# Optimization experiments

Measured on AMD Instinct MI355X. Metric: run time of the kernel, lower is better.

Reference implementation:

```python
import jax, jax.numpy as jnp
import numpy as np

B, L_IN, C_IN, C_SKIP, C_OUT, DEPTH = 8, 512, 512, 512, 512, 4
D_INNER, D_STATE, D_CONV, DT_RANK = 1024, 16, 4, 32
EPS = 1e-5


def rmsnorm(x, w):
    return x * jax.lax.rsqrt(jnp.mean(x * x, axis=-1, keepdims=True) + EPS) * w


def layernorm(x, w, b):
    m = jnp.mean(x, axis=-1, keepdims=True)
    v = jnp.mean((x - m) ** 2, axis=-1, keepdims=True)
    return (x - m) * jax.lax.rsqrt(v + EPS) * w + b


def selective_scan(u, dt, A, Bm, Cm, Dp):
    # u, dt: (B, L, Di); A: (Di, N); Bm, Cm: (B, L, N); Dp: (Di,)
    def step(h, inp):
        dt_t, B_t, C_t, u_t = inp  # (B,Di),(B,N),(B,N),(B,Di)
        dA = jnp.exp(dt_t[..., None] * A)            # (B,Di,N)
        h = dA * h + (dt_t * u_t)[..., None] * B_t[:, None, :]
        y = jnp.einsum('bdn,bn->bd', h, C_t)
        return h, y

    Bb, L, Di = u.shape
    h0 = jnp.zeros((Bb, Di, A.shape[1]), u.dtype)
    xs = (dt.transpose(1, 0, 2), Bm.transpose(1, 0, 2),
          Cm.transpose(1, 0, 2), u.transpose(1, 0, 2))
    _, ys = jax.lax.scan(step, h0, xs)               # ys: (L,B,Di)
    return ys.transpose(1, 0, 2) + u * Dp


def mamba_block(x, in_w, cw, cb, xp_w, dtw, dtb, A_log, Dp, ow, ob):
    xz = x @ in_w.T                                   # (B,L,2*Di)
    xc, z = jnp.split(xz, 2, axis=-1)
    # causal depthwise conv, kernel D_CONV
    xc_t = jax.lax.conv_general_dilated(
        xc.transpose(0, 2, 1), cw[:, None, :], (1,), [(D_CONV - 1, 0)],
        feature_group_count=D_INNER,
        dimension_numbers=('NCH', 'OIH', 'NCH'))
    xc = jax.nn.silu((xc_t + cb[None, :, None]).transpose(0, 2, 1))
    xdbc = xc @ xp_w.T                                # (B,L,DT_RANK+2N)
    dtp = xdbc[..., :DT_RANK]
    Bm = xdbc[..., DT_RANK:DT_RANK + D_STATE]
    Cm = xdbc[..., DT_RANK + D_STATE:]
    dt = jax.nn.softplus(dtp @ dtw.T + dtb)
    A = -jnp.exp(A_log)
    y = selective_scan(xc, dt, A, Bm, Cm, Dp)
    return (y * jax.nn.silu(z)) @ ow.T + ob


def forward(motion_input, skip_feats, embed, w_up, b_up, w1, b1, rms_w, w2, b2,
            ln_w, ln_b, in_proj_w, conv_w, conv_b, x_proj_w, dt_proj_w,
            dt_proj_b, A_log, D_param, out_proj_w, out_proj_b,
            norm_f_w, norm_f_b):
    Bb, Lin, C = motion_input.shape
    # ConvTranspose1d(C, C, kernel=2, stride=2): non-overlapping expansion
    up = jnp.einsum('blc,cok->blko', motion_input, w_up)
    up = up.reshape(Bb, Lin * 2, C) + b_up            # (B, 2L, C)
    x = jnp.concatenate([up, skip_feats], axis=-1)    # (B, 2L, C+skip)
    # MLP: Linear -> RMSNorm -> SiLU -> Linear
    x = jax.nn.silu(rmsnorm(x @ w1.T + b1, rms_w)) @ w2.T + b2
    # MotionMamba: add embed, depth residual mamba blocks, final norm
    x = x + embed[:, None, :]
    for i in range(DEPTH):
        x = x + mamba_block(layernorm(x, ln_w[i], ln_b[i]), in_proj_w[i],
                            conv_w[i], conv_b[i], x_proj_w[i], dt_proj_w[i],
                            dt_proj_b[i], A_log[i], D_param[i],
                            out_proj_w[i], out_proj_b[i])
    return layernorm(x, norm_f_w, norm_f_b)


def setup_inputs():
    key = jax.random.key(0)
    ks = jax.random.split(key, 16)
    f = lambda k, sh: jax.random.normal(k, sh, jnp.float32) * 0.02
    inp = {}
    inp['motion_input'] = jax.random.normal(ks[0], (B, L_IN, C_IN), jnp.float32)
    inp['skip_feats'] = jax.random.normal(ks[1], (B, 2 * L_IN, C_SKIP), jnp.float32)
    inp['embed'] = jax.random.normal(ks[2], (B, C_OUT), jnp.float32)
    inp['w_up'] = f(ks[3], (C_IN, C_IN, 2))
    inp['b_up'] = jnp.zeros((C_IN,), jnp.float32)
    inp['w1'] = f(ks[4], (C_OUT, C_IN + C_SKIP))
    inp['b1'] = jnp.zeros((C_OUT,), jnp.float32)
    inp['rms_w'] = jnp.ones((C_OUT,), jnp.float32)
    inp['w2'] = f(ks[5], (C_OUT, C_OUT))
    inp['b2'] = jnp.zeros((C_OUT,), jnp.float32)
    inp['ln_w'] = jnp.ones((DEPTH, C_OUT), jnp.float32)
    inp['ln_b'] = jnp.zeros((DEPTH, C_OUT), jnp.float32)
    inp['in_proj_w'] = f(ks[6], (DEPTH, 2 * D_INNER, C_OUT))
    inp['conv_w'] = f(ks[7], (DEPTH, D_INNER, D_CONV))
    inp['conv_b'] = jnp.zeros((DEPTH, D_INNER), jnp.float32)
    inp['x_proj_w'] = f(ks[8], (DEPTH, DT_RANK + 2 * D_STATE, D_INNER))
    inp['dt_proj_w'] = f(ks[9], (DEPTH, D_INNER, DT_RANK))
    inp['dt_proj_b'] = jnp.full((DEPTH, D_INNER), -4.0, jnp.float32)
    inp['A_log'] = jnp.log(jnp.tile(jnp.arange(1, D_STATE + 1, dtype=jnp.float32), (DEPTH, D_INNER, 1)))
    inp['D_param'] = jnp.ones((DEPTH, D_INNER), jnp.float32)
    inp['out_proj_w'] = f(ks[10], (DEPTH, C_OUT, D_INNER))
    inp['out_proj_b'] = jnp.zeros((DEPTH, C_OUT), jnp.float32)
    inp['norm_f_w'] = jnp.ones((C_OUT,), jnp.float32)
    inp['norm_f_b'] = jnp.zeros((C_OUT,), jnp.float32)
    return inp


def reference(motion_input, skip_feats, embed, w_up, b_up, w1, b1, rms_w, w2,
              b2, ln_w, ln_b, in_proj_w, conv_w, conv_b, x_proj_w, dt_proj_w,
              dt_proj_b, A_log, D_param, out_proj_w, out_proj_b,
              norm_f_w, norm_f_b):
    return forward(motion_input, skip_feats, embed, w_up, b_up, w1, b1, rms_w,
                   w2, b2, ln_w, ln_b, in_proj_w, conv_w, conv_b, x_proj_w,
                   dt_proj_w, dt_proj_b, A_log, D_param, out_proj_w,
                   out_proj_b, norm_f_w, norm_f_b)
```

## Files before the change

kernel.cpp:

```cpp
#include <hip/hip_runtime.h>
#include <cstdint>
#include <cstddef>

#define DEV_INLINE __device__ __forceinline__

static constexpr float EPS = 1e-5f;

DEV_INLINE float sigmoidf_(float x) { return 1.0f / (1.0f + __expf(-x)); }
DEV_INLINE float siluf_(float x) { return x * sigmoidf_(x); }
DEV_INLINE float softplus_fast(float x) {
    return fmaxf(x, 0.0f) + __logf(1.0f + __expf(-fabsf(x)));
}
DEV_INLINE unsigned short f2bf(float x) {
    unsigned u = __builtin_bit_cast(unsigned, x);
    u += 0x7FFFu + ((u >> 16) & 1u);
    return (unsigned short)(u >> 16);
}
DEV_INLINE float bf2f(unsigned short s) {
    unsigned u = ((unsigned)s) << 16;
    return __builtin_bit_cast(float, u);
}

typedef __attribute__((ext_vector_type(8))) short bf16x8;
typedef __attribute__((ext_vector_type(4))) float f32x4;

DEV_INLINE void gload16(const unsigned short* src, char* ldsdst) {
    __builtin_amdgcn_global_load_lds(
        (const __attribute__((address_space(1))) unsigned int*)src,
        (__attribute__((address_space(3))) unsigned int*)ldsdst, 16, 0, 0);
}

DEV_INLINE void cvt8(const float* __restrict__ s, unsigned short* __restrict__ d, int t) {
    float4 f0 = *(const float4*)(s + (size_t)t * 8);
    float4 f1 = *(const float4*)(s + (size_t)t * 8 + 4);
    union { unsigned short u[8]; uint4 v; } pk;
    pk.u[0] = f2bf(f0.x); pk.u[1] = f2bf(f0.y); pk.u[2] = f2bf(f0.z); pk.u[3] = f2bf(f0.w);
    pk.u[4] = f2bf(f1.x); pk.u[5] = f2bf(f1.y); pk.u[6] = f2bf(f1.z); pk.u[7] = f2bf(f1.w);
    *(uint4*)(d + (size_t)t * 8) = pk.v;
}

__global__ __launch_bounds__(256) void prep_all(
    const float* __restrict__ motion, const float* __restrict__ wup,
    const float* __restrict__ w1, const float* __restrict__ w2,
    const float* __restrict__ in_proj_w, const float* __restrict__ out_proj_w,
    const float* __restrict__ x_proj_w, const float* __restrict__ dt_proj_w,
    unsigned short* __restrict__ mbf, unsigned short* __restrict__ wupT,
    unsigned short* __restrict__ w1b, unsigned short* __restrict__ w2b,
    unsigned short* __restrict__ lw)
{
    int bid = (int)blockIdx.x, tid = (int)threadIdx.x;
    if (bid < 1024) {
        cvt8(motion, mbf, bid * 256 + tid);
    } else if (bid < 2048) {
        int t = (bid - 1024) * 256 + tid;
        int c = t >> 9, o = t & 511;
        float2 v = *(const float2*)(wup + (size_t)t * 2);
        wupT[(size_t)o * 512 + c] = f2bf(v.x);
        wupT[262144 + (size_t)o * 512 + c] = f2bf(v.y);
    } else if (bid < 2304) {
        cvt8(w1, w1b, (bid - 2048) * 256 + tid);
    } else if (bid < 2432) {
        cvt8(w2, w2b, (bid - 2304) * 256 + tid);
    } else {
        int r = bid - 2432;
        int layer = r / 816;
        int lb = r - layer * 816;
        unsigned short* base = lw + (size_t)layer * 1671168;
        if (lb < 512) {
            cvt8(in_proj_w + (size_t)layer * 1048576, base, lb * 256 + tid);
        } else if (lb < 768) {
            cvt8(out_proj_w + (size_t)layer * 524288, base + 1048576,
                 (lb - 512) * 256 + tid);
        } else if (lb < 800) {
            cvt8(x_proj_w + (size_t)layer * 65536, base + 1572864,
                 (lb - 768) * 256 + tid);
        } else {
            cvt8(dt_proj_w + (size_t)layer * 32768, base + 1638400,
                 (lb - 800) * 256 + tid);
        }
    }
}

template <int ACT, bool ACC, bool EMBED, bool OBF>
__global__ __launch_bounds__(256) void gemm_mfma(
    const unsigned short* __restrict__ A, int lda,
    const unsigned short* __restrict__ W, int ldw,
    void* __restrict__ Cv, int ldc, int N, int K, int gx,
    const float* __restrict__ bias, const float* __restrict__ embed)
{
    __shared__ unsigned short Asm[2][128 * 64];
    __shared__ unsigned short Wsm[2][128 * 64];
    const int tid = (int)threadIdx.x;
    const int lane = tid & 63;
    const int wv = tid >> 6;
    const int wm = wv >> 1, wn = wv & 1;

    const int nwg = (int)gridDim.x;
    const int lin = (int)blockIdx.x;
    const int logical = (lin & 7) * (nwg >> 3) + (lin >> 3);
    const int by = logical / gx;
    const int bx = logical - by * gx;
    const int bm = by * 128, bn = bx * 128;

    f32x4 acc[4][4] = {};
    const int l8 = lane >> 3;
    const int wc = lane & 7;
    const int wcg = wc ^ l8;
    const int NT = K >> 6;

    {
        char* aB = (char*)Asm[0];
        char* bB = (char*)Wsm[0];
#pragma unroll
        for (int i = 0; i < 4; ++i) {
            int rb = (i * 4 + wv) * 8;
            gload16(W + (size_t)(bn + rb + l8) * ldw + wcg * 8, bB + rb * 128);
            gload16(A + (size_t)(bm + rb + l8) * lda + wcg * 8, aB + rb * 128);
        }
    }
    __syncthreads();

    for (int t = 0; t < NT; ++t) {
        const int cur = t & 1;
        if (t + 1 < NT) {
            const int k1 = (t + 1) << 6;
            char* aB = (char*)Asm[cur ^ 1];
            char* bB = (char*)Wsm[cur ^ 1];
#pragma unroll
            for (int i = 0; i < 4; ++i) {
                int rb = (i * 4 + wv) * 8;
                gload16(W + (size_t)(bn + rb + l8) * ldw + k1 + wcg * 8, bB + rb * 128);
                gload16(A + (size_t)(bm + rb + l8) * lda + k1 + wcg * 8, aB + rb * 128);
            }
        }
        const char* aB = (const char*)Asm[cur];
        const char* bB = (const char*)Wsm[cur];
        const int rA = wm * 64 + (lane & 15);
        const int rB = wn * 64 + (lane & 15);
        const int q = lane >> 4;
#pragma unroll
        for (int kk = 0; kk < 2; ++kk) {
            bf16x8 af[4], bfr[4];
#pragma unroll
            for (int mi = 0; mi < 4; ++mi) {
                int row = rA + mi * 16;
                int ch = (kk * 4 + q) ^ (row & 7);
                af[mi] = *(const bf16x8*)(aB + row * 128 + ch * 16);
            }
#pragma unroll
            for (int ni = 0; ni < 4; ++ni) {
                int row = rB + ni * 16;
                int ch = (kk * 4 + q) ^ (row & 7);
                bfr[ni] = *(const bf16x8*)(bB + row * 128 + ch * 16);
            }
#pragma unroll
            for (int mi = 0; mi < 4; ++mi)
#pragma unroll
                for (int ni = 0; ni < 4; ++ni)
                    acc[mi][ni] = __builtin_amdgcn_mfma_f32_16x16x32_bf16(
                        af[mi], bfr[ni], acc[mi][ni], 0, 0, 0);
        }
        __syncthreads();
    }

    const int cn = lane & 15;
    const int r0 = (lane >> 4) * 4;
    const int eb = EMBED ? (bm >> 10) * N : 0;
#pragma unroll
    for (int ni = 0; ni < 4; ++ni) {
        int col = bn + wn * 64 + ni * 16 + cn;
        float add = bias ? bias[col] : 0.0f;
        if (EMBED) add += embed[eb + col];
#pragma unroll
        for (int mi = 0; mi < 4; ++mi) {
#pragma unroll
            for (int r = 0; r < 4; ++r) {
                int row = bm + wm * 64 + mi * 16 + r0 + r;
                float v = acc[mi][ni][r] + add;
                if (ACT == 1) v = softplus_fast(v);
                if (OBF) {
                    ((unsigned short*)Cv)[(size_t)row * ldc + col] = f2bf(v);
                } else {
                    float* p = (float*)Cv + (size_t)row * ldc + col;
                    if (ACC) *p += v; else *p = v;
                }
            }
        }
    }
}

template <int ACT, bool ACC, bool EMBED, bool OBF, bool UPS>
__global__ __launch_bounds__(256) void gemm_mfma64(
    const unsigned short* __restrict__ A, int lda,
    const unsigned short* __restrict__ W, int ldw,
    void* __restrict__ Cv, int ldc, int N, int K, int gx,
    const float* __restrict__ bias, const float* __restrict__ embed)
{
    __shared__ unsigned short Asm[2][64 * 64];
    __shared__ unsigned short Wsm[2][64 * 64];
    const int tid = (int)threadIdx.x;
    const int lane = tid & 63;
    const int wv = tid >> 6;
    const int wm = wv >> 1, wn = wv & 1;

    const int nwg = (int)gridDim.x;
    const int lin = (int)blockIdx.x;
    const int logical = (lin & 7) * (nwg >> 3) + (lin >> 3);
    const int by = logical / gx;
    const int bx = logical - by * gx;
    const int bm = by * 64, bn = bx * 64;

    f32x4 acc[2][2] = {};
    const int l8 = lane >> 3;
    const int wc = lane & 7;
    const int wcg = wc ^ l8;
    const int NT = K >> 6;

    {
        char* aB = (char*)Asm[0];
        char* bB = (char*)Wsm[0];
#pragma unroll
        for (int i = 0; i < 2; ++i) {
            int rb = (i * 4 + wv) * 8;
            gload16(W + (size_t)(bn + rb + l8) * ldw + wcg * 8, bB + rb * 128);
            gload16(A + (size_t)(bm + rb + l8) * lda + wcg * 8, aB + rb * 128);
        }
    }
    __syncthreads();

    for (int t = 0; t < NT; ++t) {
        const int cur = t & 1;
        if (t + 1 < NT) {
            const int k1 = (t + 1) << 6;
            char* aB = (char*)Asm[cur ^ 1];
            char* bB = (char*)Wsm[cur ^ 1];
#pragma unroll
            for (int i = 0; i < 2; ++i) {
                int rb = (i * 4 + wv) * 8;
                gload16(W + (size_t)(bn + rb + l8) * ldw + k1 + wcg * 8, bB + rb * 128);
                gload16(A + (size_t)(bm + rb + l8) * lda + k1 + wcg * 8, aB + rb * 128);
            }
        }
        const char* aB = (const char*)Asm[cur];
        const char* bB = (const char*)Wsm[cur];
        const int rA = wm * 32 + (lane & 15);
        const int rB = wn * 32 + (lane & 15);
        const int q = lane >> 4;
#pragma unroll
        for (int kk = 0; kk < 2; ++kk) {
            bf16x8 af[2], bfr[2];
#pragma unroll
            for (int mi = 0; mi < 2; ++mi) {
                int row = rA + mi * 16;
                int ch = (kk * 4 + q) ^ (row & 7);
                af[mi] = *(const bf16x8*)(aB + row * 128 + ch * 16);
            }
#pragma unroll
            for (int ni = 0; ni < 2; ++ni) {
                int row = rB + ni * 16;
                int ch = (kk * 4 + q) ^ (row & 7);
                bfr[ni] = *(const bf16x8*)(bB + row * 128 + ch * 16);
            }
#pragma unroll
            for (int mi = 0; mi < 2; ++mi)
#pragma unroll
                for (int ni = 0; ni < 2; ++ni)
                    acc[mi][ni] = __builtin_amdgcn_mfma_f32_16x16x32_bf16(
                        af[mi], bfr[ni], acc[mi][ni], 0, 0, 0);
        }
        __syncthreads();
    }

    const int cn = lane & 15;
    const int r0 = (lane >> 4) * 4;
    const int eb = EMBED ? (bm >> 10) * N : 0;
#pragma unroll
    for (int ni = 0; ni < 2; ++ni) {
        int col = bn + wn * 32 + ni * 16 + cn;
        float add = bias ? bias[UPS ? (col & 511) : col] : 0.0f;
        if (EMBED) add += embed[eb + col];
#pragma unroll
        for (int mi = 0; mi < 2; ++mi) {
#pragma unroll
            for (int r = 0; r < 4; ++r) {
                int row = bm + wm * 32 + mi * 16 + r0 + r;
                float v = acc[mi][ni][r] + add;
                if (ACT == 1) v = softplus_fast(v);
                if (UPS) {
                    size_t ad = (size_t)row * 2048 + ((col >> 9) << 10) + (col & 511);
                    ((unsigned short*)Cv)[ad] = f2bf(v);
                } else if (OBF) {
                    ((unsigned short*)Cv)[(size_t)row * ldc + col] = f2bf(v);
                } else {
                    float* p = (float*)Cv + (size_t)row * ldc + col;
                    if (ACC) *p += v; else *p = v;
                }
            }
        }
    }
}

__global__ __launch_bounds__(256) void gemm_dt(
    const unsigned short* __restrict__ xdbc,
    const unsigned short* __restrict__ wdt,
    const float* __restrict__ bias,
    unsigned short* __restrict__ out)
{
    __shared__ unsigned short S[128 * 136];
    const int tid = (int)threadIdx.x;
    const int lane = tid & 63;
    const int wv = tid >> 6;
    const int wm = wv >> 1, wn = wv & 1;

    const int lin = (int)blockIdx.x;
    const int logical = (lin & 7) * 64 + (lin >> 3);
    const int bm = (logical >> 3) * 128;
    const int bn = (logical & 7) * 128;

    const int fr = lane & 15;
    const int q = lane >> 4;

    bf16x8 af[4], wf[4];
#pragma unroll
    for (int mi = 0; mi < 4; ++mi)
        af[mi] = *(const bf16x8*)(xdbc + (size_t)(bm + wm * 64 + mi * 16 + fr) * 64 + q * 8);
#pragma unroll
    for (int ni = 0; ni < 4; ++ni)
        wf[ni] = *(const bf16x8*)(wdt + (size_t)(bn + wn * 64 + ni * 16 + fr) * 32 + q * 8);

    f32x4 acc[4][4] = {};
#pragma unroll
    for (int mi = 0; mi < 4; ++mi)
#pragma unroll
        for (int ni = 0; ni < 4; ++ni)
            acc[mi][ni] = __builtin_amdgcn_mfma_f32_16x16x32_bf16(
                af[mi], wf[ni], acc[mi][ni], 0, 0, 0);

    const int cn = lane & 15;
    const int r0 = (lane >> 4) * 4;
#pragma unroll
    for (int ni = 0; ni < 4; ++ni) {
        int lcol = wn * 64 + ni * 16 + cn;
        float add = bias[bn + lcol];
#pragma unroll
        for (int mi = 0; mi < 4; ++mi) {
#pragma unroll
            for (int r = 0; r < 4; ++r) {
                int lrow = wm * 64 + mi * 16 + r0 + r;
                S[lrow * 136 + lcol] = f2bf(softplus_fast(acc[mi][ni][r] + add));
            }
        }
    }
    __syncthreads();

    const int row = tid >> 1;
    const int half = tid & 1;
    const unsigned short* src = S + row * 136 + half * 64;
    unsigned short* dst = out + (size_t)(bm + row) * 1024 + bn + half * 64;
#pragma unroll
    for (int k = 0; k < 8; ++k) {
        uint4 v = *(const uint4*)(src + k * 8);
        *(uint4*)(dst + k * 8) = v;
    }
}

__global__ __launch_bounds__(128) void gemm_xdbc(
    const unsigned short* __restrict__ A,
    const unsigned short* __restrict__ W,
    unsigned short* __restrict__ C)
{
    __shared__ unsigned short Asm[64 * 64];
    __shared__ unsigned short Wsm[64 * 64];
    const int tid = (int)threadIdx.x;
    const int lane = tid & 63;
    const int w = tid >> 6;
    const int bm = blockIdx.x * 64;
    const int l8 = lane >> 3, wc = lane & 7, wcg = wc ^ l8;
    char* aB = (char*)Asm;
    char* bB = (char*)Wsm;

    f32x4 acc[2][4] = {};

    for (int k0 = 0; k0 < 1024; k0 += 64) {
#pragma unroll
        for (int i = 0; i < 4; ++i) {
            int rb = (i * 2 + w) * 8;
            gload16(A + (size_t)(bm + rb + l8) * 1024 + k0 + wcg * 8, aB + rb * 128);
            gload16(W + (size_t)(rb + l8) * 1024 + k0 + wcg * 8, bB + rb * 128);
        }
        __syncthreads();
        const int rA = w * 32 + (lane & 15);
        const int rB = (lane & 15);
        const int q = lane >> 4;
#pragma unroll
        for (int kk = 0; kk < 2; ++kk) {
            bf16x8 af[2], bfr[4];
#pragma unroll
            for (int mi = 0; mi < 2; ++mi) {
                int row = rA + mi * 16;
                int ch = (kk * 4 + q) ^ (row & 7);
                af[mi] = *(const bf16x8*)(aB + row * 128 + ch * 16);
            }
#pragma unroll
            for (int ni = 0; ni < 4; ++ni) {
                int row = rB + ni * 16;
                int ch = (kk * 4 + q) ^ (row & 7);
                bfr[ni] = *(const bf16x8*)(bB + row * 128 + ch * 16);
            }
#pragma unroll
            for (int mi = 0; mi < 2; ++mi)
#pragma unroll
                for (int ni = 0; ni < 4; ++ni)
                    acc[mi][ni] = __builtin_amdgcn_mfma_f32_16x16x32_bf16(
                        af[mi], bfr[ni], acc[mi][ni], 0, 0, 0);
        }
        __syncthreads();
    }
    const int cn = lane & 15;
    const int r0 = (lane >> 4) * 4;
#pragma unroll
    for (int mi = 0; mi < 2; ++mi)
#pragma unroll
        for (int ni = 0; ni < 4; ++ni)
#pragma unroll
            for (int r = 0; r < 4; ++r) {
                int row = bm + w * 32 + mi * 16 + r0 + r;
                C[(size_t)row * 64 + ni * 16 + cn] = f2bf(acc[mi][ni][r]);
            }
}

__global__ __launch_bounds__(256) void concat_skip(
    const float* __restrict__ skip, unsigned short* __restrict__ x0)
{
    int t = blockIdx.x * 256 + (int)threadIdx.x;
    int row = t >> 6;
    int c8 = (t & 63) << 3;
    const float* s = skip + (size_t)row * 512 + c8;
    float4 f0 = *(const float4*)s;
    float4 f1 = *(const float4*)(s + 4);
    union { unsigned short u[8]; uint4 v; } pk;
    pk.u[0] = f2bf(f0.x); pk.u[1] = f2bf(f0.y); pk.u[2] = f2bf(f0.z); pk.u[3] = f2bf(f0.w);
    pk.u[4] = f2bf(f1.x); pk.u[5] = f2bf(f1.y); pk.u[6] = f2bf(f1.z); pk.u[7] = f2bf(f1.w);
    *(uint4*)(x0 + (size_t)row * 1024 + 512 + c8) = pk.v;
}

template <bool BFOUT>
__global__ __launch_bounds__(256) void layernorm_k(
    const float* __restrict__ x, void* __restrict__ outp,
    const float* __restrict__ w, const float* __restrict__ b)
{
    const int row = blockIdx.x * 4 + ((int)threadIdx.x >> 6);
    const int lane = (int)threadIdx.x & 63;
    const float* xr = x + (size_t)row * 512;
    float4 v0 = *(const float4*)(xr + lane * 4);
    float4 v1 = *(const float4*)(xr + 256 + lane * 4);
    float s = v0.x + v0.y + v0.z + v0.w + v1.x + v1.y + v1.z + v1.w;
    float q = v0.x*v0.x + v0.y*v0.y + v0.z*v0.z + v0.w*v0.w
            + v1.x*v1.x + v1.y*v1.y + v1.z*v1.z + v1.w*v1.w;
#pragma unroll
    for (int o = 32; o; o >>= 1) {
        s += __shfl_xor(s, o, 64);
        q += __shfl_xor(q, o, 64);
    }
    const float mean = s * (1.0f / 512.0f);
    const float var = q * (1.0f / 512.0f) - mean * mean;
    const float rstd = rsqrtf(var + EPS);
    float4 w0 = *(const float4*)(w + lane * 4);
    float4 w1 = *(const float4*)(w + 256 + lane * 4);
    float4 b0 = *(const float4*)(b + lane * 4);
    float4 b1 = *(const float4*)(b + 256 + lane * 4);
    float4 o0, o1;
    o0.x = (v0.x - mean) * rstd * w0.x + b0.x;
    o0.y = (v0.y - mean) * rstd * w0.y + b0.y;
    o0.z = (v0.z - mean) * rstd * w0.z + b0.z;
    o0.w = (v0.w - mean) * rstd * w0.w + b0.w;
    o1.x = (v1.x - mean) * rstd * w1.x + b1.x;
    o1.y = (v1.y - mean) * rstd * w1.y + b1.y;
    o1.z = (v1.z - mean) * rstd * w1.z + b1.z;
    o1.w = (v1.w - mean) * rstd * w1.w + b1.w;
    if (BFOUT) {
        unsigned short* ob = (unsigned short*)outp + (size_t)row * 512;
        union { unsigned short u[4]; uint2 v; } p0, p1;
        p0.u[0] = f2bf(o0.x); p0.u[1] = f2bf(o0.y); p0.u[2] = f2bf(o0.z); p0.u[3] = f2bf(o0.w);
        p1.u[0] = f2bf(o1.x); p1.u[1] = f2bf(o1.y); p1.u[2] = f2bf(o1.z); p1.u[3] = f2bf(o1.w);
        *(uint2*)(ob + lane * 4) = p0.v;
        *(uint2*)(ob + 256 + lane * 4) = p1.v;
    } else {
        float* orow = (float*)outp + (size_t)row * 512;
        *(float4*)(orow + lane * 4) = o0;
        *(float4*)(orow + 256 + lane * 4) = o1;
    }
}

__global__ __launch_bounds__(256) void rms_silu_k(
    const float* __restrict__ x, unsigned short* __restrict__ o,
    const float* __restrict__ w)
{
    const int row = blockIdx.x * 4 + ((int)threadIdx.x >> 6);
    const int lane = (int)threadIdx.x & 63;
    const float* xr = x + (size_t)row * 512;
    float4 v0 = *(const float4*)(xr + lane * 4);
    float4 v1 = *(const float4*)(xr + 256 + lane * 4);
    float q = v0.x*v0.x + v0.y*v0.y + v0.z*v0.z + v0.w*v0.w
            + v1.x*v1.x + v1.y*v1.y + v1.z*v1.z + v1.w*v1.w;
#pragma unroll
    for (int of = 32; of; of >>= 1) q += __shfl_xor(q, of, 64);
    const float scale = rsqrtf(q * (1.0f / 512.0f) + EPS);
    float4 w0 = *(const float4*)(w + lane * 4);
    float4 w1 = *(const float4*)(w + 256 + lane * 4);
    union { unsigned short u[4]; uint2 v; } p0, p1;
    p0.u[0] = f2bf(siluf_(v0.x * scale * w0.x));
    p0.u[1] = f2bf(siluf_(v0.y * scale * w0.y));
    p0.u[2] = f2bf(siluf_(v0.z * scale * w0.z));
    p0.u[3] = f2bf(siluf_(v0.w * scale * w0.w));
    p1.u[0] = f2bf(siluf_(v1.x * scale * w1.x));
    p1.u[1] = f2bf(siluf_(v1.y * scale * w1.y));
    p1.u[2] = f2bf(siluf_(v1.z * scale * w1.z));
    p1.u[3] = f2bf(siluf_(v1.w * scale * w1.w));
    unsigned short* ob = o + (size_t)row * 512;
    *(uint2*)(ob + lane * 4) = p0.v;
    *(uint2*)(ob + 256 + lane * 4) = p1.v;
}

__global__ __launch_bounds__(256) void conv_silu_k2(
    const unsigned short* __restrict__ xz, unsigned short* __restrict__ ub,
    const float* __restrict__ cw, const float* __restrict__ cb)
{
    int t = blockIdx.x * 256 + (int)threadIdx.x;
    int d = t & 1023;
    int bc = t >> 10;
    int b = bc >> 4, ch = bc & 15;
    int l0 = ch * 64;
    float4 w4 = *(const float4*)(cw + (size_t)d * 4);
    float bias = cb[d];
    const unsigned short* src = xz + ((size_t)(b * 1024 + l0)) * 2048 + d;
    unsigned short* dst = ub + ((size_t)(b * 1024 + l0)) * 1024 + d;
    float x0 = 0.f, x1 = 0.f, x2 = 0.f;
    if (l0 > 0) {
        x0 = bf2f(src[-(size_t)3 * 2048]);
        x1 = bf2f(src[-(size_t)2 * 2048]);
        x2 = bf2f(src[-(size_t)1 * 2048]);
    }
    for (int l = 0; l < 64; ++l) {
        float x3 = bf2f(src[(size_t)l * 2048]);
        float v = fmaf(x0, w4.x, fmaf(x1, w4.y, fmaf(x2, w4.z, fmaf(x3, w4.w, bias))));
        dst[(size_t)l * 1024] = f2bf(siluf_(v));
        x0 = x1; x1 = x2; x2 = x3;
    }
}

template <int CTRL>
DEV_INLINE float dpp_f(float x) {
    int yi = __builtin_amdgcn_update_dpp(
        0, __builtin_bit_cast(int, x), CTRL, 0xF, 0xF, true);
    return __builtin_bit_cast(float, yi);
}

template <int PHASE>
__global__ __launch_bounds__(256) void scan6(
    const unsigned short* __restrict__ dtp,
    const unsigned short* ubf,
    unsigned short* ybf,
    const unsigned short* __restrict__ xdbc,
    const unsigned short* __restrict__ zbf,
    float* __restrict__ hp,
    const float* __restrict__ A_log,
    const float* __restrict__ Dp)
{
    __shared__ float SDT[64 * 68];
    __shared__ float SB[32][20];
    __shared__ float SC[PHASE == 2 ? 32 : 1][20];
    __shared__ float YS[PHASE == 2 ? 32 : 1][68];

    const int lin = (int)blockIdx.x;
    const int logical = (lin & 7) * 128 + (lin >> 3);
    const int gg = logical & 15;
    const int r = logical >> 4;
    const int c = r & 7, b = r >> 3;
    if (PHASE == 1 && c == 7) return;
    const int tid = (int)threadIdx.x;
    const int dl = tid >> 2, qq = tid & 3;
    const int wv = tid >> 6;
    const int lane = tid & 63;
    const int dblk = gg << 6;
    const int d = dblk + dl;
    const int m0 = b * 1024 + c * 128;

    float An[4];
#pragma unroll
    for (int j = 0; j < 4; ++j)
        An[j] = -__expf(A_log[(size_t)d * 16 + qq * 4 + j]);

    float h[4] = {};
    float prod[4] = {1.f, 1.f, 1.f, 1.f};
    if (PHASE == 2) {
        const float* hpb = hp + ((size_t)(b * 1024 + d)) * 256 + qq * 8;
        for (int cc = 0; cc < c; ++cc) {
            float4 v0 = *(const float4*)(hpb + cc * 32);
            float4 v1 = *(const float4*)(hpb + cc * 32 + 4);
            h[0] = fmaf(v0.y, h[0], v0.x);
            h[1] = fmaf(v0.w, h[1], v0.z);
            h[2] = fmaf(v1.y, h[2], v1.x);
            h[3] = fmaf(v1.w, h[3], v1.z);
        }
    }

    const int bcr = (tid & 127) >> 2;
    const int bne = (tid & 3) << 2;

    unsigned short rdt0[4], rdt1[4], ru0[4], ru1[4];
    uint2 rBC;

#pragma unroll
    for (int j = 0; j < 4; ++j) {
        size_t r0 = (size_t)(m0 + 2 * (wv * 4 + j));
        rdt0[j] = dtp[r0 * 1024 + dblk + lane];
        rdt1[j] = dtp[(r0 + 1) * 1024 + dblk + lane];
        ru0[j]  = ubf[r0 * 1024 + dblk + lane];
        ru1[j]  = ubf[(r0 + 1) * 1024 + dblk + lane];
    }
    if (tid < 128) {
        rBC = *(const uint2*)(xdbc + (size_t)(m0 + bcr) * 64 + 32 + bne);
    } else if (PHASE == 2) {
        rBC = *(const uint2*)(xdbc + (size_t)(m0 + bcr) * 64 + 48 + bne);
    }

    for (int s = 0; s < 4; ++s) {
        const int lbase = s * 32;
        if (PHASE == 1 && s > 0) __syncthreads();
#pragma unroll
        for (int j = 0; j < 4; ++j) {
            float d0 = bf2f(rdt0[j]), d1 = bf2f(rdt1[j]);
            float4 wvv = {d0, d0 * bf2f(ru0[j]), d1, d1 * bf2f(ru1[j])};
            *(float4*)&SDT[lane * 68 + (wv * 4 + j) * 4] = wvv;
        }
        if (tid < 128) {
            const unsigned short* bb = (const unsigned short*)&rBC;
            float4 bv = {bf2f(bb[0]), bf2f(bb[1]), bf2f(bb[2]), bf2f(bb[3])};
            *(float4*)&SB[bcr][bne] = bv;
        } else if (PHASE == 2) {
            const unsigned short* cc2 = (const unsigned short*)&rBC;
            float4 cv = {bf2f(cc2[0]), bf2f(cc2[1]), bf2f(cc2[2]), bf2f(cc2[3])};
            *(float4*)&SC[bcr][bne] = cv;
        }
        if (s < 3) {
            const int nb = lbase + 32;
#pragma unroll
            for (int j = 0; j < 4; ++j) {
                size_t r0 = (size_t)(m0 + nb + 2 * (wv * 4 + j));
                rdt0[j] = dtp[r0 * 1024 + dblk + lane];
                rdt1[j] = dtp[(r0 + 1) * 1024 + dblk + lane];
                ru0[j]  = ubf[r0 * 1024 + dblk + lane];
                ru1[j]  = ubf[(r0 + 1) * 1024 + dblk + lane];
            }
            if (tid < 128) {
                rBC = *(const uint2*)(xdbc + (size_t)(m0 + nb + bcr) * 64 + 32 + bne);
            } else if (PHASE == 2) {
                rBC = *(const uint2*)(xdbc + (size_t)(m0 + nb + bcr) * 64 + 48 + bne);
            }
        }
        __syncthreads();

        for (int l2 = 0; l2 < 16; ++l2) {
            float4 sd = *(const float4*)&SDT[dl * 68 + l2 * 4];
            float4 B0 = *(const float4*)&SB[2 * l2][qq * 4];
            float4 B1 = *(const float4*)&SB[2 * l2 + 1][qq * 4];
            float p0 = 0.0f, p1 = 0.0f;
            float4 C0, C1;
            if (PHASE == 2) {
                C0 = *(const float4*)&SC[2 * l2][qq * 4];
                C1 = *(const float4*)&SC[2 * l2 + 1][qq * 4];
            }
            const float* B0p = (const float*)&B0;
            const float* B1p = (const float*)&B1;
            const float* C0p = (const float*)&C0;
            const float* C1p = (const float*)&C1;
#pragma unroll
            for (int j = 0; j < 4; ++j) {
                float e0 = __expf(sd.x * An[j]);
                if (PHASE == 1) prod[j] *= e0;
                h[j] = fmaf(e0, h[j], sd.y * B0p[j]);
                if (PHASE == 2) p0 = fmaf(h[j], C0p[j], p0);
                float e1 = __expf(sd.z * An[j]);
                if (PHASE == 1) prod[j] *= e1;
                h[j] = fmaf(e1, h[j], sd.w * B1p[j]);
                if (PHASE == 2) p1 = fmaf(h[j], C1p[j], p1);
            }
            if (PHASE == 2) {
                p0 += dpp_f<0xB1>(p0);
                p0 += dpp_f<0x4E>(p0);
                p1 += dpp_f<0xB1>(p1);
                p1 += dpp_f<0x4E>(p1);
                if (qq == 0) {
                    YS[2 * l2][dl] = p0;
                    YS[2 * l2 + 1][dl] = p1;
                }
            }
        }

        if (PHASE == 2) {
            __syncthreads();
            const int row = tid >> 3;
            const int e8 = (tid & 7) * 8;
            size_t gr = (size_t)(m0 + lbase + row);
            float4 p40 = *(const float4*)&YS[row][e8];
            float4 p41 = *(const float4*)&YS[row][e8 + 4];
            uint4 uu = *(const uint4*)(ubf + gr * 1024 + dblk + e8);
            uint4 zz = *(const uint4*)(zbf + gr * 2048 + 1024 + dblk + e8);
            float4 D0 = *(const float4*)(Dp + dblk + e8);
            float4 D1 = *(const float4*)(Dp + dblk + e8 + 4);
            const unsigned short* up = (const unsigned short*)&uu;
            const unsigned short* zp = (const unsigned short*)&zz;
            const float* pp0 = (const float*)&p40;
            const float* pp1 = (const float*)&p41;
            const float* dd0 = (const float*)&D0;
            const float* dd1 = (const float*)&D1;
            union { unsigned short u[8]; uint4 v; } pk;
#pragma unroll
            for (int j = 0; j < 4; ++j) {
                float y = fmaf(bf2f(up[j]), dd0[j], pp0[j]) * siluf_(bf2f(zp[j]));
                pk.u[j] = f2bf(y);
            }
#pragma unroll
            for (int j = 0; j < 4; ++j) {
                float y = fmaf(bf2f(up[4 + j]), dd1[j], pp1[j]) * siluf_(bf2f(zp[4 + j]));
                pk.u[4 + j] = f2bf(y);
            }
            __syncthreads();
            *(uint4*)(ybf + gr * 1024 + dblk + e8) = pk.v;
        }
    }

    if (PHASE == 1) {
        float* hpo = hp + ((size_t)(b * 1024 + d)) * 256 + c * 32 + qq * 8;
        float4 o0 = {h[0], prod[0], h[1], prod[1]};
        float4 o1 = {h[2], prod[2], h[3], prod[3]};
        *(float4*)hpo = o0;
        *(float4*)(hpo + 4) = o1;
    }
}

extern "C" void kernel_launch(void* const* d_in, const int* in_sizes, int n_in,
                              void* d_out, int out_size, void* d_ws, size_t ws_size,
                              hipStream_t stream)
{
    const float* motion     = (const float*)d_in[0];
    const float* skip       = (const float*)d_in[1];
    const float* embed      = (const float*)d_in[2];
    const float* w_up       = (const float*)d_in[3];
    const float* b_up       = (const float*)d_in[4];
    const float* w1         = (const float*)d_in[5];
    const float* b1         = (const float*)d_in[6];
    const float* rms_w      = (const float*)d_in[7];
    const float* w2         = (const float*)d_in[8];
    const float* b2         = (const float*)d_in[9];
    const float* ln_w       = (const float*)d_in[10];
    const float* ln_b       = (const float*)d_in[11];
    const float* in_proj_w  = (const float*)d_in[12];
    const float* conv_w     = (const float*)d_in[13];
    const float* conv_b     = (const float*)d_in[14];
    const float* x_proj_w   = (const float*)d_in[15];
    const float* dt_proj_w  = (const float*)d_in[16];
    const float* dt_proj_b  = (const float*)d_in[17];
    const float* A_log      = (const float*)d_in[18];
    const float* D_param    = (const float*)d_in[19];
    const float* out_proj_w = (const float*)d_in[20];
    const float* out_proj_b = (const float*)d_in[21];
    const float* norm_f_w   = (const float*)d_in[22];
    const float* norm_f_b   = (const float*)d_in[23];
    float* out = (float*)d_out;
    float* ws = (float*)d_ws;

    float* xbuf = ws;
    float* xlnf = ws + 4194304;
    unsigned short* xzbf  = (unsigned short*)(ws + 8388608);
    unsigned short* ubf   = (unsigned short*)(ws + 16777216);
    unsigned short* dtybf = (unsigned short*)(ws + 20971520);
    unsigned short* xdbc  = (unsigned short*)(ws + 25165824);
    float* hp  = ws + 25427968;
    unsigned short* xsbf = (unsigned short*)(ws + 29622272);
    unsigned short* mbf  = (unsigned short*)(ws + 31719424);
    unsigned short* wupT = (unsigned short*)(ws + 32768000);
    unsigned short* w1b  = (unsigned short*)(ws + 33030144);
    unsigned short* w2b  = (unsigned short*)(ws + 33292288);
    unsigned short* lw   = (unsigned short*)(ws + 33423360);

    unsigned short* x0bf = xzbf;

    dim3 blk(256);

    prep_all<<<dim3(5696), blk, 0, stream>>>(
        motion, w_up, w1, w2, in_proj_w, out_proj_w, x_proj_w, dt_proj_w,
        mbf, wupT, w1b, w2b, lw);

    gemm_mfma64<0, false, false, true, true><<<dim3(1024), blk, 0, stream>>>(
        mbf, 512, wupT, 512, x0bf, 0, 1024, 512, 16, b_up, nullptr);
    concat_skip<<<dim3(2048), blk, 0, stream>>>(skip, x0bf);

    gemm_mfma64<0, false, false, false, false><<<dim3(1024), blk, 0, stream>>>(
        x0bf, 1024, w1b, 1024, xlnf, 512, 512, 1024, 8, b1, nullptr);
    rms_silu_k<<<dim3(2048), blk, 0, stream>>>(xlnf, xsbf, rms_w);

    gemm_mfma64<0, false, true, false, false><<<dim3(1024), blk, 0, stream>>>(
        xsbf, 512, w2b, 512, xbuf, 512, 512, 512, 8, b2, embed);

    for (int i = 0; i < 4; ++i) {
        unsigned short* ipw = lw + (size_t)i * 1671168;
        unsigned short* opw = ipw + 1048576;
        unsigned short* xpw = ipw + 1572864;
        unsigned short* wdt = ipw + 1638400;
        layernorm_k<true><<<dim3(2048), blk, 0, stream>>>(
            xbuf, xsbf, ln_w + (size_t)i * 512, ln_b + (size_t)i * 512);
        gemm_mfma<0, false, false, true><<<dim3(1024), blk, 0, stream>>>(
            xsbf, 512, ipw, 512, xzbf, 2048, 2048, 512, 16, nullptr, nullptr);
        conv_silu_k2<<<dim3(512), blk, 0, stream>>>(
            xzbf, ubf, conv_w + (size_t)i * 4096, conv_b + (size_t)i * 1024);
        gemm_xdbc<<<dim3(128), dim3(128), 0, stream>>>(ubf, xpw, xdbc);
        gemm_dt<<<dim3(512), blk, 0, stream>>>(
            xdbc, wdt, dt_proj_b + (size_t)i * 1024, dtybf);
        scan6<1><<<dim3(1024), blk, 0, stream>>>(
            dtybf, ubf, nullptr, xdbc, xzbf, hp,
            A_log + (size_t)i * 16384, D_param + (size_t)i * 1024);
        scan6<2><<<dim3(1024), blk, 0, stream>>>(
            dtybf, ubf, ubf, xdbc, xzbf, hp,
            A_log + (size_t)i * 16384, D_param + (size_t)i * 1024);
        gemm_mfma64<0, true, false, false, false><<<dim3(1024), blk, 0, stream>>>(
            ubf, 1024, opw, 1024, xbuf, 512, 512, 1024, 8,
            out_proj_b + (size_t)i * 512, nullptr);
    }

    layernorm_k<false><<<dim3(2048), blk, 0, stream>>>(xbuf, out, norm_f_w, norm_f_b);
}
```

Baseline: 698.6 us.

## Halve scan block size to 32 channels per block with vectorized staging loads

The two-phase chunked selective scan now uses 128-thread blocks that each cover 32 inner channels instead of 256 threads over 64, which doubles the grid to 2048 blocks. The dt and u staging loads become 8-byte vector loads per thread, transposed into a padded shared tile with stride 70. Each thread now loads both B and C instead of splitting them across thread halves. The aim is more blocks in flight and fewer scalar global loads for this latency-bound scan, at the cost of more per-block overhead and repeated B/C loads across blocks.

```diff
diff --git a/kernel.cpp b/kernel.cpp
--- a/kernel.cpp
+++ b/kernel.cpp
@@ -557,7 +557,7 @@
 }
 
 template <int PHASE>
-__global__ __launch_bounds__(256) void scan6(
+__global__ __launch_bounds__(128) void scan7(
     const unsigned short* __restrict__ dtp,
     const unsigned short* ubf,
     unsigned short* ybf,
@@ -567,22 +567,20 @@
     const float* __restrict__ A_log,
     const float* __restrict__ Dp)
 {
-    __shared__ float SDT[64 * 68];
+    __shared__ float SDT[32 * 70];
     __shared__ float SB[32][20];
     __shared__ float SC[PHASE == 2 ? 32 : 1][20];
-    __shared__ float YS[PHASE == 2 ? 32 : 1][68];
+    __shared__ float YS[PHASE == 2 ? 32 : 1][36];
 
     const int lin = (int)blockIdx.x;
-    const int logical = (lin & 7) * 128 + (lin >> 3);
-    const int gg = logical & 15;
-    const int r = logical >> 4;
+    const int logical = (lin & 7) * 256 + (lin >> 3);
+    const int g = logical & 31;
+    const int r = logical >> 5;
     const int c = r & 7, b = r >> 3;
     if (PHASE == 1 && c == 7) return;
     const int tid = (int)threadIdx.x;
     const int dl = tid >> 2, qq = tid & 3;
-    const int wv = tid >> 6;
-    const int lane = tid & 63;
-    const int dblk = gg << 6;
+    const int dblk = g << 5;
     const int d = dblk + dl;
     const int m0 = b * 1024 + c * 128;
 
@@ -605,64 +603,69 @@
         }
     }
 
-    const int bcr = (tid & 127) >> 2;
+    const int sr = tid >> 3;
+    const int sg = (tid & 7) * 4;
+    const int bcr = tid >> 2;
     const int bne = (tid & 3) << 2;
 
-    unsigned short rdt0[4], rdt1[4], ru0[4], ru1[4];
-    uint2 rBC;
-
-#pragma unroll
-    for (int j = 0; j < 4; ++j) {
-        size_t r0 = (size_t)(m0 + 2 * (wv * 4 + j));
-        rdt0[j] = dtp[r0 * 1024 + dblk + lane];
-        rdt1[j] = dtp[(r0 + 1) * 1024 + dblk + lane];
-        ru0[j]  = ubf[r0 * 1024 + dblk + lane];
-        ru1[j]  = ubf[(r0 + 1) * 1024 + dblk + lane];
-    }
-    if (tid < 128) {
-        rBC = *(const uint2*)(xdbc + (size_t)(m0 + bcr) * 64 + 32 + bne);
-    } else if (PHASE == 2) {
-        rBC = *(const uint2*)(xdbc + (size_t)(m0 + bcr) * 64 + 48 + bne);
+    uint2 rd0, rd1, ru0, ru1, rB, rC;
+
+    {
+        size_t ra = (size_t)(m0 + sr);
+        size_t rb2 = (size_t)(m0 + 16 + sr);
+        rd0 = *(const uint2*)(dtp + ra * 1024 + dblk + sg);
+        rd1 = *(const uint2*)(dtp + rb2 * 1024 + dblk + sg);
+        ru0 = *(const uint2*)(ubf + ra * 1024 + dblk + sg);
+        ru1 = *(const uint2*)(ubf + rb2 * 1024 + dblk + sg);
+        rB = *(const uint2*)(xdbc + (size_t)(m0 + bcr) * 64 + 32 + bne);
+        if (PHASE == 2)
+            rC = *(const uint2*)(xdbc + (size_t)(m0 + bcr) * 64 + 48 + bne);
     }
 
     for (int s = 0; s < 4; ++s) {
         const int lbase = s * 32;
         if (PHASE == 1 && s > 0) __syncthreads();
-#pragma unroll
-        for (int j = 0; j < 4; ++j) {
-            float d0 = bf2f(rdt0[j]), d1 = bf2f(rdt1[j]);
-            float4 wvv = {d0, d0 * bf2f(ru0[j]), d1, d1 * bf2f(ru1[j])};
-            *(float4*)&SDT[lane * 68 + (wv * 4 + j) * 4] = wvv;
-        }
-        if (tid < 128) {
-            const unsigned short* bb = (const unsigned short*)&rBC;
+        {
+            const unsigned short* dp0 = (const unsigned short*)&rd0;
+            const unsigned short* dp1 = (const unsigned short*)&rd1;
+            const unsigned short* up0 = (const unsigned short*)&ru0;
+            const unsigned short* up1 = (const unsigned short*)&ru1;
+            const int l20 = sr >> 1, hh = (sr & 1) * 2;
+            const int l21 = (16 + sr) >> 1;
+#pragma unroll
+            for (int j = 0; j < 4; ++j) {
+                float d0 = bf2f(dp0[j]);
+                float2 v0 = {d0, d0 * bf2f(up0[j])};
+                *(float2*)&SDT[(sg + j) * 70 + l20 * 4 + hh] = v0;
+                float d1 = bf2f(dp1[j]);
+                float2 v1 = {d1, d1 * bf2f(up1[j])};
+                *(float2*)&SDT[(sg + j) * 70 + l21 * 4 + hh] = v1;
+            }
+            const unsigned short* bb = (const unsigned short*)&rB;
             float4 bv = {bf2f(bb[0]), bf2f(bb[1]), bf2f(bb[2]), bf2f(bb[3])};
             *(float4*)&SB[bcr][bne] = bv;
-        } else if (PHASE == 2) {
-            const unsigned short* cc2 = (const unsigned short*)&rBC;
-            float4 cv = {bf2f(cc2[0]), bf2f(cc2[1]), bf2f(cc2[2]), bf2f(cc2[3])};
-            *(float4*)&SC[bcr][bne] = cv;
+            if (PHASE == 2) {
+                const unsigned short* cp = (const unsigned short*)&rC;
+                float4 cv = {bf2f(cp[0]), bf2f(cp[1]), bf2f(cp[2]), bf2f(cp[3])};
+                *(float4*)&SC[bcr][bne] = cv;
+            }
         }
         if (s < 3) {
             const int nb = lbase + 32;
-#pragma unroll
-            for (int j = 0; j < 4; ++j) {
-                size_t r0 = (size_t)(m0 + nb + 2 * (wv * 4 + j));
-                rdt0[j] = dtp[r0 * 1024 + dblk + lane];
-                rdt1[j] = dtp[(r0 + 1) * 1024 + dblk + lane];
-                ru0[j]  = ubf[r0 * 1024 + dblk + lane];
-                ru1[j]  = ubf[(r0 + 1) * 1024 + dblk + lane];
-            }
-            if (tid < 128) {
-                rBC = *(const uint2*)(xdbc + (size_t)(m0 + nb + bcr) * 64 + 32 + bne);
-            } else if (PHASE == 2) {
-                rBC = *(const uint2*)(xdbc + (size_t)(m0 + nb + bcr) * 64 + 48 + bne);
-            }
+            size_t ra = (size_t)(m0 + nb + sr);
+            size_t rb2 = (size_t)(m0 + nb + 16 + sr);
+            rd0 = *(const uint2*)(dtp + ra * 1024 + dblk + sg);
+            rd1 = *(const uint2*)(dtp + rb2 * 1024 + dblk + sg);
+            ru0 = *(const uint2*)(ubf + ra * 1024 + dblk + sg);
+            ru1 = *(const uint2*)(ubf + rb2 * 1024 + dblk + sg);
+            rB = *(const uint2*)(xdbc + (size_t)(m0 + nb + bcr) * 64 + 32 + bne);
+            if (PHASE == 2)
+                rC = *(const uint2*)(xdbc + (size_t)(m0 + nb + bcr) * 64 + 48 + bne);
         }
         __syncthreads();
 
         for (int l2 = 0; l2 < 16; ++l2) {
-            float4 sd = *(const float4*)&SDT[dl * 68 + l2 * 4];
+            float4 sd = *(const float4*)&SDT[dl * 70 + l2 * 4];
             float4 B0 = *(const float4*)&SB[2 * l2][qq * 4];
             float4 B1 = *(const float4*)&SB[2 * l2 + 1][qq * 4];
             float p0 = 0.0f, p1 = 0.0f;
@@ -700,15 +703,15 @@
 
         if (PHASE == 2) {
             __syncthreads();
-            const int row = tid >> 3;
-            const int e8 = (tid & 7) * 8;
+            const int row = tid >> 2;
+            const int d8 = (tid & 3) * 8;
             size_t gr = (size_t)(m0 + lbase + row);
-            float4 p40 = *(const float4*)&YS[row][e8];
-            float4 p41 = *(const float4*)&YS[row][e8 + 4];
-            uint4 uu = *(const uint4*)(ubf + gr * 1024 + dblk + e8);
-            uint4 zz = *(const uint4*)(zbf + gr * 2048 + 1024 + dblk + e8);
-            float4 D0 = *(const float4*)(Dp + dblk + e8);
-            float4 D1 = *(const float4*)(Dp + dblk + e8 + 4);
+            float4 p40 = *(const float4*)&YS[row][d8];
+            float4 p41 = *(const float4*)&YS[row][d8 + 4];
+            uint4 uu = *(const uint4*)(ubf + gr * 1024 + dblk + d8);
+            uint4 zz = *(const uint4*)(zbf + gr * 2048 + 1024 + dblk + d8);
+            float4 D0 = *(const float4*)(Dp + dblk + d8);
+            float4 D1 = *(const float4*)(Dp + dblk + d8 + 4);
             const unsigned short* up = (const unsigned short*)&uu;
             const unsigned short* zp = (const unsigned short*)&zz;
             const float* pp0 = (const float*)&p40;
@@ -727,7 +730,7 @@
                 pk.u[4 + j] = f2bf(y);
             }
             __syncthreads();
-            *(uint4*)(ybf + gr * 1024 + dblk + e8) = pk.v;
+            *(uint4*)(ybf + gr * 1024 + dblk + d8) = pk.v;
         }
     }
 
@@ -818,10 +821,10 @@
         gemm_xdbc<<<dim3(128), dim3(128), 0, stream>>>(ubf, xpw, xdbc);
         gemm_dt<<<dim3(512), blk, 0, stream>>>(
             xdbc, wdt, dt_proj_b + (size_t)i * 1024, dtybf);
-        scan6<1><<<dim3(1024), blk, 0, stream>>>(
+        scan7<1><<<dim3(2048), dim3(128), 0, stream>>>(
             dtybf, ubf, nullptr, xdbc, xzbf, hp,
             A_log + (size_t)i * 16384, D_param + (size_t)i * 1024);
-        scan6<2><<<dim3(1024), blk, 0, stream>>>(
+        scan7<2><<<dim3(2048), dim3(128), 0, stream>>>(
             dtybf, ubf, ubf, xdbc, xzbf, hp,
             A_log + (size_t)i * 16384, D_param + (size_t)i * 1024);
         gemm_mfma64<0, true, false, false, false><<<dim3(1024), blk, 0, stream>>>(
```

Measured after the change: 694.7 us. Within noise of the previous version (-0.6%).
